# Optimization experiments

Hardware: AMD Instinct MI355X
Metric: run time of the kernel (lower is better)

## Reference

```python
import jax, jax.numpy as jnp
import numpy as np

B, T, N, F_DIM = 8, 32, 64, 6
D, H, C = 128, 4, 32          # hidden, spatial heads, head dim
L_SP, L_T, TH = 3, 3, 4       # spatial layers, temporal layers, temporal heads
THD = D // TH                 # temporal head dim
E = N * (N - 1)


def _ln(x, g, b, eps=1e-5):
    mu = x.mean(-1, keepdims=True)
    var = ((x - mu) ** 2).mean(-1, keepdims=True)
    return (x - mu) * jax.lax.rsqrt(var + eps) * g + b


def setup_inputs() -> dict:
    key = jax.random.key(0)
    ks = iter(jax.random.split(key, 64))
    r = lambda *s: jax.random.normal(next(ks), s, jnp.float32) * 0.05
    src_n, dst_n = np.nonzero(~np.eye(N, dtype=bool))
    inp = {
        'input_frames': jax.random.normal(next(ks), (B, T, N, F_DIM), jnp.float32),
        'edge_attr_seq': jax.random.uniform(next(ks), (B, T, E, 1), jnp.float32),
        'proj_W': r(F_DIM, D), 'proj_b': r(D),
        'sp_Wq': r(L_SP, D, D), 'sp_bq': r(L_SP, D),
        'sp_Wk': r(L_SP, D, D), 'sp_bk': r(L_SP, D),
        'sp_Wv': r(L_SP, D, D), 'sp_bv': r(L_SP, D),
        'sp_We': r(L_SP, 1, D), 'sp_be': r(L_SP, D),
        'sp_Ws': r(L_SP, D, D), 'sp_bs': r(L_SP, D),
        'sp_lng': jnp.ones((L_SP, D), jnp.float32), 'sp_lnb': jnp.zeros((L_SP, D), jnp.float32),
        'temporal_pos': r(1, 512, D),
        't_Wqkv': r(L_T, D, 3 * D), 't_bqkv': r(L_T, 3 * D),
        't_Wo': r(L_T, D, D), 't_bo': r(L_T, D),
        't_ln1g': jnp.ones((L_T, D), jnp.float32), 't_ln1b': jnp.zeros((L_T, D), jnp.float32),
        't_W1': r(L_T, D, 4 * D), 't_b1': r(L_T, 4 * D),
        't_W2': r(L_T, 4 * D, D), 't_b2': r(L_T, D),
        't_ln2g': jnp.ones((L_T, D), jnp.float32), 't_ln2b': jnp.zeros((L_T, D), jnp.float32),
        'head_W1': r(D, D), 'head_b1': r(D),
        'head_W2': r(D, F_DIM), 'head_b2': r(F_DIM),
        'edge_index': jnp.asarray(np.stack([src_n, dst_n]), jnp.int32),
    }
    return inp


def _forward(input_frames, edge_attr_seq, proj_W, proj_b, sp_Wq, sp_bq, sp_Wk, sp_bk,
             sp_Wv, sp_bv, sp_We, sp_be, sp_Ws, sp_bs, sp_lng, sp_lnb, temporal_pos,
             t_Wqkv, t_bqkv, t_Wo, t_bo, t_ln1g, t_ln1b, t_W1, t_b1, t_W2, t_b2,
             t_ln2g, t_ln2b, head_W1, head_b1, head_W2, head_b2, edge_index):
    BT = B * T
    Nt = BT * N                                       # total batched nodes
    offs = jnp.arange(BT, dtype=edge_index.dtype) * N
    src = (edge_index[0][None, :] + offs[:, None]).reshape(-1)   # (BT*E,)
    dst = (edge_index[1][None, :] + offs[:, None]).reshape(-1)
    ea = edge_attr_seq.reshape(BT * E, 1)
    h = input_frames.reshape(Nt, F_DIM) @ proj_W + proj_b        # (Nt, D)

    scale = 1.0 / jnp.sqrt(jnp.float32(C))
    for l in range(L_SP):
        q = (h @ sp_Wq[l] + sp_bq[l]).reshape(Nt, H, C)
        k = (h @ sp_Wk[l] + sp_bk[l]).reshape(Nt, H, C)
        v = (h @ sp_Wv[l] + sp_bv[l]).reshape(Nt, H, C)
        e = (ea @ sp_We[l] + sp_be[l]).reshape(-1, H, C)         # (Et, H, C)
        kj = k[src] + e
        alpha = (q[dst] * kj).sum(-1) * scale                    # (Et, H)
        amax = jax.ops.segment_max(alpha, dst, num_segments=Nt)
        ae = jnp.exp(alpha - amax[dst])
        asum = jax.ops.segment_sum(ae, dst, num_segments=Nt)
        w = ae / asum[dst]                                       # segment softmax
        msg = (v[src] + e) * w[..., None]
        agg = jax.ops.segment_sum(msg, dst, num_segments=Nt).reshape(Nt, D)
        out = agg + h @ sp_Ws[l] + sp_bs[l]                      # root/skip term
        h = _ln(h + out, sp_lng[l], sp_lnb[l])

    z = h.reshape(B, T, N, D).transpose(0, 2, 1, 3).reshape(B * N, T, D)
    z = z + temporal_pos[:, :T, :]

    causal = jnp.tril(jnp.ones((T, T), bool))
    tscale = 1.0 / jnp.sqrt(jnp.float32(THD))
    for l in range(L_T):
        qkv = z @ t_Wqkv[l] + t_bqkv[l]
        q, k, v = jnp.split(qkv, 3, axis=-1)
        q = q.reshape(B * N, T, TH, THD)
        k = k.reshape(B * N, T, TH, THD)
        v = v.reshape(B * N, T, TH, THD)
        s = jnp.einsum('bqhd,bkhd->bhqk', q, k) * tscale
        s = jnp.where(causal, s, -jnp.inf)
        a = jax.nn.softmax(s, axis=-1)
        o = jnp.einsum('bhqk,bkhd->bqhd', a, v).reshape(B * N, T, D)
        o = o @ t_Wo[l] + t_bo[l]
        z = _ln(z + o, t_ln1g[l], t_ln1b[l])
        f = jax.nn.gelu(z @ t_W1[l] + t_b1[l], approximate=False) @ t_W2[l] + t_b2[l]
        z = _ln(z + f, t_ln2g[l], t_ln2b[l])

    h_last = z[:, -1, :].reshape(B, N, D)
    pred = jax.nn.gelu(h_last @ head_W1 + head_b1, approximate=False) @ head_W2 + head_b2
    return pred                                                  # (B, N, F)


def reference(input_frames, edge_attr_seq, proj_W, proj_b, sp_Wq, sp_bq, sp_Wk, sp_bk,
              sp_Wv, sp_bv, sp_We, sp_be, sp_Ws, sp_bs, sp_lng, sp_lnb, temporal_pos,
              t_Wqkv, t_bqkv, t_Wo, t_bo, t_ln1g, t_ln1b, t_W1, t_b1, t_W2, t_b2,
              t_ln2g, t_ln2b, head_W1, head_b1, head_W2, head_b2, edge_index):
    return _forward(input_frames, edge_attr_seq, proj_W, proj_b, sp_Wq, sp_bq, sp_Wk,
                    sp_bk, sp_Wv, sp_bv, sp_We, sp_be, sp_Ws, sp_bs, sp_lng, sp_lnb,
                    temporal_pos, t_Wqkv, t_bqkv, t_Wo, t_bo, t_ln1g, t_ln1b, t_W1,
                    t_b1, t_W2, t_b2, t_ln2g, t_ln2b, head_W1, head_b1, head_W2,
                    head_b2, edge_index)
```

## Files before the change

kernel.cpp:

```cpp
#include <hip/hip_runtime.h>
#include <hip/hip_bf16.h>
#include <math.h>

typedef __hip_bfloat16 bf16;
typedef short short8 __attribute__((ext_vector_type(8)));
typedef float floatx4 __attribute__((ext_vector_type(4)));

#define B_    8
#define T_    32
#define N_    64
#define F_    6
#define D_    128
#define E_    4032
#define BT_   256
#define BN_   512

__device__ __forceinline__ float gelu_exact(float x) {
    return 0.5f * x * (1.0f + erff(x * 0.70710678118654752f));
}
__device__ __forceinline__ float bfbits2f(short s) {
    unsigned int u = ((unsigned int)(unsigned short)s) << 16;
    return __uint_as_float(u);
}
__device__ __forceinline__ void ld32lds(const bf16* p, float* o) {
    const short8* sp = (const short8*)p;
#pragma unroll
    for (int i = 0; i < 4; i++) {
        short8 s = sp[i];
#pragma unroll
        for (int j = 0; j < 8; j++) o[i * 8 + j] = bfbits2f(s[j]);
    }
}

struct RepackDesc { const float* W; bf16* out; int K, N, ntt, ntoff, L, start; };
struct RepackArgs {
    RepackDesc d[9]; int total;
    const float *bq, *bk, *bv; float* spb;
};

__global__ void k_repack(RepackArgs ra) {
    int gid = blockIdx.x * blockDim.x + threadIdx.x;
    if (gid >= ra.total) {
        int i = gid - ra.total;
        if (i < 3 * 384) {
            int l = i / 384, c = i % 384;
            float v = (c < 128) ? ra.bq[l * 128 + c]
                    : (c < 256) ? ra.bk[l * 128 + c - 128]
                                : ra.bv[l * 128 + c - 256];
            ra.spb[i] = v;
        }
        return;
    }
    int fi = 0;
    while (fi < 8 && gid >= ra.d[fi + 1].start) fi++;
    RepackDesc dd = ra.d[fi];
    int r = gid - dd.start;
    int lane = r & 63; r >>= 6;
    int ntiles = dd.N >> 4;
    int nt = r % ntiles; r /= ntiles;
    int ktiles = dd.K >> 5;
    int kt = r % ktiles;
    int l = r / ktiles;
    int quad = lane >> 4, cc = lane & 15;
    const float* Wl = dd.W + (size_t)l * dd.K * dd.N;
    bf16* o = dd.out + ((((size_t)l * ktiles + kt) * dd.ntt + nt + dd.ntoff) * 64 + lane) * 8;
    int kb = kt * 32 + quad * 8;
    int n = nt * 16 + cc;
#pragma unroll
    for (int j = 0; j < 8; j++)
        o[j] = __float2bfloat16(Wl[(size_t)(kb + j) * dd.N + n]);
}

__global__ __launch_bounds__(512, 1)
void k_spatial3(const float* __restrict__ inp, const float* __restrict__ projW,
                const float* __restrict__ projB,
                const short8* __restrict__ BpQKV, const short8* __restrict__ BpWS,
                const float* __restrict__ spb, const float* __restrict__ bs,
                const float* __restrict__ lng, const float* __restrict__ lnb,
                const float* __restrict__ ea, const float* __restrict__ Weg,
                const float* __restrict__ beg, const float* __restrict__ tpos,
                float* __restrict__ z32g) {
    __shared__ short smem[61312];
    bf16* hb = (bf16*)smem;
    bf16* qk = (bf16*)(smem + 8704);
    float* aggf = (float*)(smem + 8704);
    float* fsm = (float*)(smem + 8704);
    bf16* Vt = (bf16*)(smem + 25600);
    bf16* Ps = (bf16*)(smem + 34816);
    float* EAs = (float*)(smem + 53248);

    int bt = blockIdx.x;
    int tid = threadIdx.x;
    int lane = tid & 63, w = tid >> 6;
    int quad = lane >> 4, col = lane & 15;
    int w4 = w & 3, wh = w >> 2;
    const float scale = 0.17677669529663687f;

    for (int i = tid; i < 896; i += 512)
        fsm[i] = (i < 768) ? projW[i] : projB[i - 768];
    {
        const float* eag = ea + (size_t)bt * E_;
        for (int i = tid; i < E_; i += 512) EAs[i] = eag[i];
    }
    __syncthreads();
    float hreg[32];
    if (w < 4) {
#pragma unroll
        for (int r = 0; r < 4; r++) {
            int n = w * 16 + quad * 4 + r;
            const float* xr = inp + (size_t)(bt * 64 + n) * F_;
            float xin[6];
#pragma unroll
            for (int k2 = 0; k2 < 6; k2++) xin[k2] = xr[k2];
#pragma unroll
            for (int tt = 0; tt < 8; tt++) {
                int c = tt * 16 + col;
                float a = fsm[768 + c];
#pragma unroll
                for (int k2 = 0; k2 < 6; k2++) a = fmaf(xin[k2], fsm[k2 * 128 + c], a);
                hreg[tt * 4 + r] = a;
                hb[n * 136 + c] = __float2bfloat16(a);
            }
        }
    }
    __syncthreads();

    for (int l = 0; l < 3; l++) {
        {
            floatx4 acc[12];
#pragma unroll
            for (int tt = 0; tt < 12; tt++) acc[tt] = (floatx4){0.f, 0.f, 0.f, 0.f};
            const short8* bpl = BpQKV + (size_t)l * 6144;
            for (int kt = 0; kt < 4; kt++) {
                short8 a = *(const short8*)&hb[(w4 * 16 + col) * 136 + kt * 32 + quad * 8];
                const short8* bp = bpl + (size_t)(kt * 24 + wh * 12) * 64 + lane;
#pragma unroll
                for (int tt = 0; tt < 12; tt++)
                    acc[tt] = __builtin_amdgcn_mfma_f32_16x16x32_bf16(a, bp[tt * 64], acc[tt], 0, 0, 0);
            }
            const float* bias = spb + l * 384;
#pragma unroll
            for (int tt = 0; tt < 12; tt++) {
                int c = wh * 192 + tt * 16 + col;
                float bv = bias[c];
#pragma unroll
                for (int r = 0; r < 4; r++) {
                    int row = w4 * 16 + quad * 4 + r;
                    bf16 v = __float2bfloat16(acc[tt][r] + bv);
                    if (c < 256) qk[row * 264 + c] = v;
                    else         Vt[(c - 256) * 72 + row] = v;
                }
            }
        }
        __syncthreads();
        int h = w4, half = wh;
        int hoff = h * 32;
        const float* Wel = Weg + l * 128 + hoff;
        const float* bel = beg + l * 128 + hoff;
        float qWe;
        {
            int dst = half * 32 + (lane & 31);
            float qr[32];
            ld32lds(&qk[dst * 264 + hoff], qr);
            float s0 = 0.f, s1 = 0.f, s2 = 0.f, s3 = 0.f;
#pragma unroll
            for (int c2 = 0; c2 < 32; c2 += 4) {
                s0 = fmaf(qr[c2], Wel[c2], s0);
                s1 = fmaf(qr[c2 + 1], Wel[c2 + 1], s1);
                s2 = fmaf(qr[c2 + 2], Wel[c2 + 2], s2);
                s3 = fmaf(qr[c2 + 3], Wel[c2 + 3], s3);
            }
            qWe = (s0 + s1) + (s2 + s3);
        }
        float s[2][4][4], ev[2][4][4];
        {
            short8 aA[2], bB[4];
#pragma unroll
            for (int mtl = 0; mtl < 2; mtl++)
                aA[mtl] = *(const short8*)&qk[((half * 2 + mtl) * 16 + col) * 264 + hoff + quad * 8];
#pragma unroll
            for (int nt = 0; nt < 4; nt++)
                bB[nt] = *(const short8*)&qk[(nt * 16 + col) * 264 + 128 + hoff + quad * 8];
#pragma unroll
            for (int mtl = 0; mtl < 2; mtl++)
#pragma unroll
                for (int nt = 0; nt < 4; nt++) {
                    floatx4 acc = (floatx4){0.f, 0.f, 0.f, 0.f};
                    acc = __builtin_amdgcn_mfma_f32_16x16x32_bf16(aA[mtl], bB[nt], acc, 0, 0, 0);
#pragma unroll
                    for (int r = 0; r < 4; r++) s[mtl][nt][r] = acc[r];
                }
        }
        __syncthreads();
        float ls[2][4], ae[2][4], inv[2][4];
#pragma unroll
        for (int mtl = 0; mtl < 2; mtl++)
#pragma unroll
            for (int r = 0; r < 4; r++) {
                int m = half * 32 + mtl * 16 + quad * 4 + r;
                float qWeR = __shfl(qWe, mtl * 16 + quad * 4 + r, 64);
                float rmax = -1e30f;
#pragma unroll
                for (int nt = 0; nt < 4; nt++) {
                    int n = nt * 16 + col;
                    bool diag = (m == n);
                    int eid = diag ? 0 : (n * 63 + m - (m > n ? 1 : 0));
                    float eav = diag ? 0.f : EAs[eid];
                    ev[mtl][nt][r] = eav;
                    float al = diag ? -1e30f
                                    : scale * (s[mtl][nt][r] + eav * qWeR);
                    s[mtl][nt][r] = al;
                    rmax = fmaxf(rmax, al);
                }
#pragma unroll
                for (int mk2 = 1; mk2 <= 8; mk2 <<= 1)
                    rmax = fmaxf(rmax, __shfl_xor(rmax, mk2, 64));
                float lsum = 0.f, aesum = 0.f;
#pragma unroll
                for (int nt = 0; nt < 4; nt++) {
                    float p = __expf(s[mtl][nt][r] - rmax);
                    s[mtl][nt][r] = p;
                    lsum += p;
                    aesum = fmaf(p, ev[mtl][nt][r], aesum);
                }
#pragma unroll
                for (int mk2 = 1; mk2 <= 8; mk2 <<= 1) {
                    lsum += __shfl_xor(lsum, mk2, 64);
                    aesum += __shfl_xor(aesum, mk2, 64);
                }
                ls[mtl][r] = lsum;
                ae[mtl][r] = aesum;
                inv[mtl][r] = 1.0f / lsum;
            }
        bf16* PsH = Ps + h * 4608;
        floatx4 oacc[2][2];
#pragma unroll
        for (int mtl = 0; mtl < 2; mtl++)
#pragma unroll
            for (int ntB = 0; ntB < 2; ntB++) oacc[mtl][ntB] = (floatx4){0.f, 0.f, 0.f, 0.f};
#pragma unroll
        for (int p = 0; p < 2; p++) {
#pragma unroll
            for (int mtl = 0; mtl < 2; mtl++)
#pragma unroll
                for (int q2 = 0; q2 < 2; q2++) {
                    int nl = q2 * 16 + col;
                    int base0 = (half * 32 + mtl * 16 + quad * 4) * 72 + ((nl >> 3) * 2) * 8 + (nl & 7);
#pragma unroll
                    for (int r = 0; r < 4; r++) {
                        float p_ = s[mtl][2 * p + q2][r];
                        bf16 hi = __float2bfloat16(p_);
                        bf16 lo = __float2bfloat16(p_ - bfbits2f(*(short*)&hi));
                        PsH[base0 + r * 72] = hi;
                        PsH[base0 + r * 72 + 8] = lo;
                    }
                }
            short8 aPh[2], aPl[2], bV[2];
#pragma unroll
            for (int mtl = 0; mtl < 2; mtl++) {
                int rb = (half * 32 + mtl * 16 + col) * 72 + quad * 16;
                aPh[mtl] = *(const short8*)&PsH[rb];
                aPl[mtl] = *(const short8*)&PsH[rb + 8];
            }
#pragma unroll
            for (int ntB = 0; ntB < 2; ntB++)
                bV[ntB] = *(const short8*)&Vt[(hoff + ntB * 16 + col) * 72 + p * 32 + quad * 8];
#pragma unroll
            for (int mtl = 0; mtl < 2; mtl++)
#pragma unroll
                for (int ntB = 0; ntB < 2; ntB++) {
                    oacc[mtl][ntB] = __builtin_amdgcn_mfma_f32_16x16x32_bf16(aPh[mtl], bV[ntB], oacc[mtl][ntB], 0, 0, 0);
                    oacc[mtl][ntB] = __builtin_amdgcn_mfma_f32_16x16x32_bf16(aPl[mtl], bV[ntB], oacc[mtl][ntB], 0, 0, 0);
                }
        }
#pragma unroll
        for (int mtl = 0; mtl < 2; mtl++)
#pragma unroll
            for (int ntB = 0; ntB < 2; ntB++) {
                int c = hoff + ntB * 16 + col;
                float Wc = Wel[ntB * 16 + col];
                float bc = bel[ntB * 16 + col];
#pragma unroll
                for (int r = 0; r < 4; r++) {
                    int m = half * 32 + mtl * 16 + quad * 4 + r;
                    aggf[m * 128 + c] = fmaf(fmaf(ae[mtl][r], Wc, oacc[mtl][ntB][r]),
                                             inv[mtl][r], bc);
                }
            }
        __syncthreads();
        if (w < 4) {
            floatx4 acc2[8];
#pragma unroll
            for (int tt = 0; tt < 8; tt++) acc2[tt] = (floatx4){0.f, 0.f, 0.f, 0.f};
            const short8* bpl = BpWS + (size_t)l * 2048;
            for (int kt = 0; kt < 4; kt++) {
                short8 a = *(const short8*)&hb[(w * 16 + col) * 136 + kt * 32 + quad * 8];
                const short8* bp = bpl + (size_t)(kt * 8) * 64 + lane;
#pragma unroll
                for (int tt = 0; tt < 8; tt++)
                    acc2[tt] = __builtin_amdgcn_mfma_f32_16x16x32_bf16(a, bp[tt * 64], acc2[tt], 0, 0, 0);
            }
            const float* bsl = bs + l * 128;
            float vv[32], rs[4] = {0.f, 0.f, 0.f, 0.f};
#pragma unroll
            for (int tt = 0; tt < 8; tt++) {
                int c = tt * 16 + col;
                float bv = bsl[c];
#pragma unroll
                for (int r = 0; r < 4; r++) {
                    int row = w * 16 + quad * 4 + r;
                    float v = acc2[tt][r] + bv + aggf[row * 128 + c] + hreg[tt * 4 + r];
                    vv[tt * 4 + r] = v;
                    rs[r] += v;
                }
            }
#pragma unroll
            for (int m = 1; m <= 8; m <<= 1)
#pragma unroll
                for (int r = 0; r < 4; r++) rs[r] += __shfl_xor(rs[r], m, 64);
            float mean[4], vs[4] = {0.f, 0.f, 0.f, 0.f};
#pragma unroll
            for (int r = 0; r < 4; r++) mean[r] = rs[r] * (1.0f / 128.0f);
#pragma unroll
            for (int i = 0; i < 32; i++) {
                float d = vv[i] - mean[i & 3];
                vv[i] = d;
                vs[i & 3] += d * d;
            }
#pragma unroll
            for (int m = 1; m <= 8; m <<= 1)
#pragma unroll
                for (int r = 0; r < 4; r++) vs[r] += __shfl_xor(vs[r], m, 64);
            float inv2[4];
#pragma unroll
            for (int r = 0; r < 4; r++) inv2[r] = rsqrtf(vs[r] * (1.0f / 128.0f) + 1e-5f);
            const float* gl = lng + l * 128;
            const float* bl = lnb + l * 128;
            if (l < 2) {
#pragma unroll
                for (int tt = 0; tt < 8; tt++) {
                    int c = tt * 16 + col;
                    float gc = gl[c], bc = bl[c];
#pragma unroll
                    for (int r = 0; r < 4; r++) {
                        float y = vv[tt * 4 + r] * inv2[r] * gc + bc;
                        int n = w * 16 + quad * 4 + r;
                        hreg[tt * 4 + r] = y;
                        hb[n * 136 + c] = __float2bfloat16(y);
                    }
                }
            } else {
                int b = bt >> 5, t_ = bt & 31;
#pragma unroll
                for (int tt = 0; tt < 8; tt++) {
                    int c = tt * 16 + col;
                    float gc = gl[c], bc = bl[c], pc = tpos[t_ * 128 + c];
#pragma unroll
                    for (int r = 0; r < 4; r++) {
                        float y = vv[tt * 4 + r] * inv2[r] * gc + bc;
                        int n = w * 16 + quad * 4 + r;
                        z32g[((size_t)(b * 64 + n) * 32 + t_) * 128 + c] = y + pc;
                    }
                }
            }
        }
        __syncthreads();
    }
}

__global__ __launch_bounds__(512, 4)
void k_temporal3(const float* __restrict__ z32g,
                 const short8* __restrict__ BpQKV, const short8* __restrict__ BpWO,
                 const short8* __restrict__ BpW1, const short8* __restrict__ BpW2,
                 const float* __restrict__ bqkv, const float* __restrict__ bo,
                 const float* __restrict__ ln1g, const float* __restrict__ ln1b,
                 const float* __restrict__ b1, const float* __restrict__ b2,
                 const float* __restrict__ ln2g, const float* __restrict__ ln2b,
                 bf16* __restrict__ zlastb) {
    __shared__ short smem[32000];
    bf16* zb  = (bf16*)smem;
    bf16* qk  = (bf16*)(smem + 4352);
    bf16* Ps  = (bf16*)(smem + 12800);
    bf16* Vt  = (bf16*)(smem + 22016);
    bf16* o16 = (bf16*)(smem + 27136);
    float* lnp = (float*)(smem + 31488);
    bf16* f1  = (bf16*)(smem + 4352);

    int bn = blockIdx.x;
    int tid = threadIdx.x;
    int lane = tid & 63, w = tid >> 6;
    int quad = lane >> 4, col = lane & 15;
    int mt = w & 1, cq = w >> 1;
    const float scale = 0.17677669529663687f;

    for (int i = tid; i < 4096; i += 512) {
        float v = z32g[(size_t)bn * 4096 + i];
        zb[(i >> 7) * 136 + (i & 127)] = __float2bfloat16(v);
    }
    float zreg[8];
#pragma unroll
    for (int t2 = 0; t2 < 2; t2++)
#pragma unroll
        for (int r = 0; r < 4; r++)
            zreg[t2 * 4 + r] = z32g[(size_t)bn * 4096 +
                                    (mt * 16 + quad * 4 + r) * 128 + cq * 32 + t2 * 16 + col];
    __syncthreads();

    for (int l = 0; l < 3; l++) {
        {
            floatx4 acc[6];
#pragma unroll
            for (int tt = 0; tt < 6; tt++) acc[tt] = (floatx4){0.f, 0.f, 0.f, 0.f};
            const short8* bpl = BpQKV + (size_t)l * 6144;
            for (int kt = 0; kt < 4; kt++) {
                short8 a = *(const short8*)&zb[(mt * 16 + col) * 136 + kt * 32 + quad * 8];
                const short8* bp = bpl + (size_t)(kt * 24 + cq * 6) * 64 + lane;
#pragma unroll
                for (int tt = 0; tt < 6; tt++)
                    acc[tt] = __builtin_amdgcn_mfma_f32_16x16x32_bf16(a, bp[tt * 64], acc[tt], 0, 0, 0);
            }
            const float* bias = bqkv + l * 384;
#pragma unroll
            for (int tt = 0; tt < 6; tt++) {
                int c = cq * 96 + tt * 16 + col;
                float bv = bias[c];
#pragma unroll
                for (int r = 0; r < 4; r++) {
                    int row = mt * 16 + quad * 4 + r;
                    bf16 v = __float2bfloat16(acc[tt][r] + bv);
                    if (c < 256) qk[row * 264 + c] = v;
                    else         Vt[(c - 256) * 40 + row] = v;
                }
            }
        }
        __syncthreads();
        {
            int h = w & 3, mh = w >> 2;
            int hoff = h * 32;
            bf16* PsH = Ps + (h * 2 + mh) * 1152;
            float s[2][4];
            short8 aA = *(const short8*)&qk[(mh * 16 + col) * 264 + hoff + quad * 8];
            short8 bB[2];
#pragma unroll
            for (int nt = 0; nt < 2; nt++)
                bB[nt] = *(const short8*)&qk[(nt * 16 + col) * 264 + 128 + hoff + quad * 8];
#pragma unroll
            for (int nt = 0; nt < 2; nt++) {
                floatx4 acc = (floatx4){0.f, 0.f, 0.f, 0.f};
                acc = __builtin_amdgcn_mfma_f32_16x16x32_bf16(aA, bB[nt], acc, 0, 0, 0);
#pragma unroll
                for (int r = 0; r < 4; r++) s[nt][r] = acc[r];
            }
            float inv[4];
#pragma unroll
            for (int r = 0; r < 4; r++) {
                int m = mh * 16 + quad * 4 + r;
                float rmax = -1e30f;
#pragma unroll
                for (int nt = 0; nt < 2; nt++) {
                    int n = nt * 16 + col;
                    float al = (n > m) ? -1e30f : s[nt][r] * scale;
                    s[nt][r] = al;
                    rmax = fmaxf(rmax, al);
                }
#pragma unroll
                for (int mk2 = 1; mk2 <= 8; mk2 <<= 1)
                    rmax = fmaxf(rmax, __shfl_xor(rmax, mk2, 64));
                float lsum = 0.f;
#pragma unroll
                for (int nt = 0; nt < 2; nt++) {
                    float p = __expf(s[nt][r] - rmax);
                    s[nt][r] = p;
                    lsum += p;
                }
#pragma unroll
                for (int mk2 = 1; mk2 <= 8; mk2 <<= 1)
                    lsum += __shfl_xor(lsum, mk2, 64);
                inv[r] = 1.0f / lsum;
            }
#pragma unroll
            for (int nt = 0; nt < 2; nt++) {
                int n = nt * 16 + col;
                int base0 = (quad * 4) * 72 + ((n >> 3) * 2) * 8 + (n & 7);
#pragma unroll
                for (int r = 0; r < 4; r++) {
                    float p_ = s[nt][r];
                    bf16 hi = __float2bfloat16(p_);
                    bf16 lo = __float2bfloat16(p_ - bfbits2f(*(short*)&hi));
                    PsH[base0 + r * 72] = hi;
                    PsH[base0 + r * 72 + 8] = lo;
                }
            }
            floatx4 oacc[2];
#pragma unroll
            for (int nt = 0; nt < 2; nt++) oacc[nt] = (floatx4){0.f, 0.f, 0.f, 0.f};
            short8 aPh = *(const short8*)&PsH[col * 72 + quad * 16];
            short8 aPl = *(const short8*)&PsH[col * 72 + quad * 16 + 8];
            short8 bV[2];
#pragma unroll
            for (int nt = 0; nt < 2; nt++)
                bV[nt] = *(const short8*)&Vt[(hoff + nt * 16 + col) * 40 + quad * 8];
#pragma unroll
            for (int nt = 0; nt < 2; nt++) {
                oacc[nt] = __builtin_amdgcn_mfma_f32_16x16x32_bf16(aPh, bV[nt], oacc[nt], 0, 0, 0);
                oacc[nt] = __builtin_amdgcn_mfma_f32_16x16x32_bf16(aPl, bV[nt], oacc[nt], 0, 0, 0);
            }
#pragma unroll
            for (int nt = 0; nt < 2; nt++) {
                int c = hoff + nt * 16 + col;
#pragma unroll
                for (int r = 0; r < 4; r++)
                    o16[(mh * 16 + quad * 4 + r) * 136 + c] =
                        __float2bfloat16(oacc[nt][r] * inv[r]);
            }
        }
        __syncthreads();
        {
            floatx4 acc2[2];
#pragma unroll
            for (int tt = 0; tt < 2; tt++) acc2[tt] = (floatx4){0.f, 0.f, 0.f, 0.f};
            const short8* bpl = BpWO + (size_t)l * 2048;
            for (int kt = 0; kt < 4; kt++) {
                short8 a = *(const short8*)&o16[(mt * 16 + col) * 136 + kt * 32 + quad * 8];
                const short8* bp = bpl + (size_t)(kt * 8 + cq * 2) * 64 + lane;
#pragma unroll
                for (int tt = 0; tt < 2; tt++)
                    acc2[tt] = __builtin_amdgcn_mfma_f32_16x16x32_bf16(a, bp[tt * 64], acc2[tt], 0, 0, 0);
            }
            const float* bol = bo + l * 128;
            float vv[8], rs[4] = {0.f, 0.f, 0.f, 0.f}, rq[4] = {0.f, 0.f, 0.f, 0.f};
#pragma unroll
            for (int tt = 0; tt < 2; tt++) {
                int c = cq * 32 + tt * 16 + col;
                float bv = bol[c];
#pragma unroll
                for (int r = 0; r < 4; r++) {
                    float v = acc2[tt][r] + bv + zreg[tt * 4 + r];
                    vv[tt * 4 + r] = v;
                    rs[r] += v;
                    rq[r] = fmaf(v, v, rq[r]);
                }
            }
#pragma unroll
            for (int m = 1; m <= 8; m <<= 1)
#pragma unroll
                for (int r = 0; r < 4; r++) {
                    rs[r] += __shfl_xor(rs[r], m, 64);
                    rq[r] += __shfl_xor(rq[r], m, 64);
                }
            if (col == 0) {
#pragma unroll
                for (int r = 0; r < 4; r++) {
                    int row = mt * 16 + quad * 4 + r;
                    lnp[(cq * 32 + row) * 2] = rs[r];
                    lnp[(cq * 32 + row) * 2 + 1] = rq[r];
                }
            }
            __syncthreads();
            const float* gl = ln1g + l * 128;
            const float* bl = ln1b + l * 128;
#pragma unroll
            for (int r = 0; r < 4; r++) {
                int row = mt * 16 + quad * 4 + r;
                float sm = 0.f, sq = 0.f;
#pragma unroll
                for (int q2 = 0; q2 < 4; q2++) {
                    sm += lnp[(q2 * 32 + row) * 2];
                    sq += lnp[(q2 * 32 + row) * 2 + 1];
                }
                float mean = sm * (1.0f / 128.0f);
                float var = sq * (1.0f / 128.0f) - mean * mean;
                float iv = rsqrtf(var + 1e-5f);
#pragma unroll
                for (int tt = 0; tt < 2; tt++) {
                    int c = cq * 32 + tt * 16 + col;
                    float y = (vv[tt * 4 + r] - mean) * iv * gl[c] + bl[c];
                    zreg[tt * 4 + r] = y;
                    zb[row * 136 + c] = __float2bfloat16(y);
                }
            }
        }
        __syncthreads();
        {
            floatx4 acc3[8];
#pragma unroll
            for (int tt = 0; tt < 8; tt++) acc3[tt] = (floatx4){0.f, 0.f, 0.f, 0.f};
            const short8* bpl = BpW1 + (size_t)l * 8192;
            for (int kt = 0; kt < 4; kt++) {
                short8 a = *(const short8*)&zb[(mt * 16 + col) * 136 + kt * 32 + quad * 8];
                const short8* bp = bpl + (size_t)(kt * 32 + cq * 8) * 64 + lane;
#pragma unroll
                for (int tt = 0; tt < 8; tt++)
                    acc3[tt] = __builtin_amdgcn_mfma_f32_16x16x32_bf16(a, bp[tt * 64], acc3[tt], 0, 0, 0);
            }
            const float* b1l = b1 + l * 512;
#pragma unroll
            for (int tt = 0; tt < 8; tt++) {
                int c = cq * 128 + tt * 16 + col;
                float bv = b1l[c];
#pragma unroll
                for (int r = 0; r < 4; r++) {
                    float v = gelu_exact(acc3[tt][r] + bv);
                    f1[(mt * 16 + quad * 4 + r) * 520 + c] = __float2bfloat16(v);
                }
            }
        }
        __syncthreads();
        {
            floatx4 acc4[2];
#pragma unroll
            for (int tt = 0; tt < 2; tt++) acc4[tt] = (floatx4){0.f, 0.f, 0.f, 0.f};
            const short8* bpl = BpW2 + (size_t)l * 8192;
            for (int kt = 0; kt < 16; kt++) {
                short8 a = *(const short8*)&f1[(mt * 16 + col) * 520 + kt * 32 + quad * 8];
                const short8* bp = bpl + (size_t)(kt * 8 + cq * 2) * 64 + lane;
#pragma unroll
                for (int tt = 0; tt < 2; tt++)
                    acc4[tt] = __builtin_amdgcn_mfma_f32_16x16x32_bf16(a, bp[tt * 64], acc4[tt], 0, 0, 0);
            }
            const float* b2l = b2 + l * 128;
            float vv[8], rs[4] = {0.f, 0.f, 0.f, 0.f}, rq[4] = {0.f, 0.f, 0.f, 0.f};
#pragma unroll
            for (int tt = 0; tt < 2; tt++) {
                int c = cq * 32 + tt * 16 + col;
                float bv = b2l[c];
#pragma unroll
                for (int r = 0; r < 4; r++) {
                    float v = acc4[tt][r] + bv + zreg[tt * 4 + r];
                    vv[tt * 4 + r] = v;
                    rs[r] += v;
                    rq[r] = fmaf(v, v, rq[r]);
                }
            }
#pragma unroll
            for (int m = 1; m <= 8; m <<= 1)
#pragma unroll
                for (int r = 0; r < 4; r++) {
                    rs[r] += __shfl_xor(rs[r], m, 64);
                    rq[r] += __shfl_xor(rq[r], m, 64);
                }
            if (col == 0) {
#pragma unroll
                for (int r = 0; r < 4; r++) {
                    int row = mt * 16 + quad * 4 + r;
                    lnp[(cq * 32 + row) * 2] = rs[r];
                    lnp[(cq * 32 + row) * 2 + 1] = rq[r];
                }
            }
            __syncthreads();
            const float* gl = ln2g + l * 128;
            const float* bl = ln2b + l * 128;
#pragma unroll
            for (int r = 0; r < 4; r++) {
                int row = mt * 16 + quad * 4 + r;
                float sm = 0.f, sq = 0.f;
#pragma unroll
                for (int q2 = 0; q2 < 4; q2++) {
                    sm += lnp[(q2 * 32 + row) * 2];
                    sq += lnp[(q2 * 32 + row) * 2 + 1];
                }
                float mean = sm * (1.0f / 128.0f);
                float var = sq * (1.0f / 128.0f) - mean * mean;
                float iv = rsqrtf(var + 1e-5f);
#pragma unroll
                for (int tt = 0; tt < 2; tt++) {
                    int c = cq * 32 + tt * 16 + col;
                    float y = (vv[tt * 4 + r] - mean) * iv * gl[c] + bl[c];
                    zreg[tt * 4 + r] = y;
                    if (l < 2) zb[row * 136 + c] = __float2bfloat16(y);
                    else if (row == 31) zlastb[(size_t)bn * 128 + c] = __float2bfloat16(y);
                }
            }
        }
        __syncthreads();
    }
}

__global__ __launch_bounds__(256)
void k_head(const bf16* __restrict__ zlastb, const short8* __restrict__ BpHW1,
            const float* __restrict__ b1, const float* __restrict__ W2,
            const float* __restrict__ b2, float* __restrict__ out) {
    __shared__ bf16 h1[16 * 136];
    int blk = blockIdx.x;
    int tid = threadIdx.x;
    int lane = tid & 63, w = tid >> 6;
    int quad = lane >> 4, col = lane & 15;
    {
        floatx4 acc[2];
        acc[0] = (floatx4){0.f, 0.f, 0.f, 0.f};
        acc[1] = (floatx4){0.f, 0.f, 0.f, 0.f};
        const short8* Ap = (const short8*)(zlastb + (size_t)(blk * 16 + col) * 128) + quad;
        for (int kt = 0; kt < 4; kt++) {
            short8 a = Ap[kt * 4];
            const short8* bp = BpHW1 + (size_t)(kt * 8 + w * 2) * 64 + lane;
            acc[0] = __builtin_amdgcn_mfma_f32_16x16x32_bf16(a, bp[0], acc[0], 0, 0, 0);
            acc[1] = __builtin_amdgcn_mfma_f32_16x16x32_bf16(a, bp[64], acc[1], 0, 0, 0);
        }
#pragma unroll
        for (int tt = 0; tt < 2; tt++) {
            int c = w * 32 + tt * 16 + col;
            float bv = b1[c];
#pragma unroll
            for (int r = 0; r < 4; r++)
                h1[(quad * 4 + r) * 136 + c] = __float2bfloat16(gelu_exact(acc[tt][r] + bv));
        }
    }
    __syncthreads();
    if (tid < 96) {
        int row = tid / 6, c = tid % 6;
        float a0 = 0.f, a1 = 0.f, a2 = 0.f, a3 = 0.f;
        const bf16* hr = &h1[row * 136];
#pragma unroll 8
        for (int k = 0; k < 128; k += 4) {
            a0 = fmaf(bfbits2f(*(const short*)&hr[k]),     W2[k * 6 + c], a0);
            a1 = fmaf(bfbits2f(*(const short*)&hr[k + 1]), W2[(k + 1) * 6 + c], a1);
            a2 = fmaf(bfbits2f(*(const short*)&hr[k + 2]), W2[(k + 2) * 6 + c], a2);
            a3 = fmaf(bfbits2f(*(const short*)&hr[k + 3]), W2[(k + 3) * 6 + c], a3);
        }
        out[(size_t)(blk * 16 + row) * 6 + c] = (a0 + a1) + (a2 + a3) + b2[c];
    }
}

extern "C" void kernel_launch(void* const* d_in, const int* in_sizes, int n_in,
                              void* d_out, int out_size, void* d_ws, size_t ws_size,
                              hipStream_t stream) {
    const float* input_frames = (const float*)d_in[0];
    const float* edge_attr    = (const float*)d_in[1];
    const float* proj_W  = (const float*)d_in[2];
    const float* proj_b  = (const float*)d_in[3];
    const float* sp_Wq   = (const float*)d_in[4];
    const float* sp_bq   = (const float*)d_in[5];
    const float* sp_Wk   = (const float*)d_in[6];
    const float* sp_bk   = (const float*)d_in[7];
    const float* sp_Wv   = (const float*)d_in[8];
    const float* sp_bv   = (const float*)d_in[9];
    const float* sp_We   = (const float*)d_in[10];
    const float* sp_be   = (const float*)d_in[11];
    const float* sp_Ws   = (const float*)d_in[12];
    const float* sp_bs   = (const float*)d_in[13];
    const float* sp_lng  = (const float*)d_in[14];
    const float* sp_lnb  = (const float*)d_in[15];
    const float* tpos    = (const float*)d_in[16];
    const float* t_Wqkv  = (const float*)d_in[17];
    const float* t_bqkv  = (const float*)d_in[18];
    const float* t_Wo    = (const float*)d_in[19];
    const float* t_bo    = (const float*)d_in[20];
    const float* t_ln1g  = (const float*)d_in[21];
    const float* t_ln1b  = (const float*)d_in[22];
    const float* t_W1    = (const float*)d_in[23];
    const float* t_b1    = (const float*)d_in[24];
    const float* t_W2    = (const float*)d_in[25];
    const float* t_b2    = (const float*)d_in[26];
    const float* t_ln2g  = (const float*)d_in[27];
    const float* t_ln2b  = (const float*)d_in[28];
    const float* head_W1 = (const float*)d_in[29];
    const float* head_b1 = (const float*)d_in[30];
    const float* head_W2 = (const float*)d_in[31];
    const float* head_b2 = (const float*)d_in[32];

    float* f     = (float*)d_ws;
    float* z32g  = f;
    bf16*  zlastb = (bf16*)(f + (1u << 21));
    float* spb   = f + (1u << 21) + 65536;
    bf16* BpBase = (bf16*)(f + (1u << 21) + 65536 + 2048);
    bf16* BpSPQKV = BpBase;
    bf16* BpWS    = BpSPQKV + 147456;
    bf16* BpTQKV  = BpWS + 49152;
    bf16* BpWO    = BpTQKV + 147456;
    bf16* BpW1    = BpWO + 49152;
    bf16* BpW2    = BpW1 + 196608;
    bf16* BpHW1   = BpW2 + 196608;

    RepackArgs ra;
    int s = 0;
    auto mk = [&](int i, const float* W, bf16* out, int K, int N, int ntt, int ntoff, int L) {
        ra.d[i] = {W, out, K, N, ntt, ntoff, L, s};
        s += L * (K >> 5) * (N >> 4) * 64;
    };
    mk(0, sp_Wq, BpSPQKV, 128, 128, 24, 0, 3);
    mk(1, sp_Wk, BpSPQKV, 128, 128, 24, 8, 3);
    mk(2, sp_Wv, BpSPQKV, 128, 128, 24, 16, 3);
    mk(3, sp_Ws, BpWS, 128, 128, 8, 0, 3);
    mk(4, t_Wqkv, BpTQKV, 128, 384, 24, 0, 3);
    mk(5, t_Wo, BpWO, 128, 128, 8, 0, 3);
    mk(6, t_W1, BpW1, 128, 512, 32, 0, 3);
    mk(7, t_W2, BpW2, 512, 128, 8, 0, 3);
    mk(8, head_W1, BpHW1, 128, 128, 8, 0, 1);
    ra.total = s;
    ra.bq = sp_bq; ra.bk = sp_bk; ra.bv = sp_bv; ra.spb = spb;
    k_repack<<<(s + 1152 + 255) / 256, 256, 0, stream>>>(ra);

    k_spatial3<<<BT_, 512, 0, stream>>>(
        input_frames, proj_W, proj_b,
        (const short8*)BpSPQKV, (const short8*)BpWS,
        spb, sp_bs, sp_lng, sp_lnb, edge_attr, sp_We, sp_be, tpos, z32g);

    k_temporal3<<<BN_, 512, 0, stream>>>(
        z32g, (const short8*)BpTQKV, (const short8*)BpWO,
        (const short8*)BpW1, (const short8*)BpW2,
        t_bqkv, t_bo, t_ln1g, t_ln1b, t_b1, t_b2, t_ln2g, t_ln2b, zlastb);

    k_head<<<32, 256, 0, stream>>>(zlastb, (const short8*)BpHW1, head_b1,
                                   head_W2, head_b2, (float*)d_out);
}
```

Before: 279.9 us.

## Process two sequences per temporal block to reuse weight fragments across both

```diff
diff --git a/kernel.cpp b/kernel.cpp
--- a/kernel.cpp
+++ b/kernel.cpp
@@ -368,7 +368,7 @@
     }
 }
 
-__global__ __launch_bounds__(512, 4)
+__global__ __launch_bounds__(512, 2)
 void k_temporal3(const float* __restrict__ z32g,
                  const short8* __restrict__ BpQKV, const short8* __restrict__ BpWO,
                  const short8* __restrict__ BpW1, const short8* __restrict__ BpW2,
@@ -377,47 +377,57 @@
                  const float* __restrict__ b1, const float* __restrict__ b2,
                  const float* __restrict__ ln2g, const float* __restrict__ ln2b,
                  bf16* __restrict__ zlastb) {
-    __shared__ short smem[32000];
+    __shared__ short smem[64000];
     bf16* zb  = (bf16*)smem;
-    bf16* qk  = (bf16*)(smem + 4352);
-    bf16* Ps  = (bf16*)(smem + 12800);
-    bf16* Vt  = (bf16*)(smem + 22016);
-    bf16* o16 = (bf16*)(smem + 27136);
-    float* lnp = (float*)(smem + 31488);
-    bf16* f1  = (bf16*)(smem + 4352);
-
-    int bn = blockIdx.x;
+    bf16* qk  = (bf16*)(smem + 8704);
+    bf16* Ps  = (bf16*)(smem + 25600);
+    bf16* Vt  = (bf16*)(smem + 44032);
+    bf16* o16 = (bf16*)(smem + 54272);
+    float* lnp = (float*)(smem + 62976);
+    bf16* f1  = (bf16*)(smem + 8704);
+
+    int bn0 = blockIdx.x * 2;
     int tid = threadIdx.x;
     int lane = tid & 63, w = tid >> 6;
     int quad = lane >> 4, col = lane & 15;
-    int mt = w & 1, cq = w >> 1;
+    int sq = w & 1, cq = w >> 1;
     const float scale = 0.17677669529663687f;
 
-    for (int i = tid; i < 4096; i += 512) {
-        float v = z32g[(size_t)bn * 4096 + i];
-        zb[(i >> 7) * 136 + (i & 127)] = __float2bfloat16(v);
+    for (int i = tid; i < 8192; i += 512) {
+        int s = i >> 12, j = i & 4095;
+        float v = z32g[(size_t)(bn0 + s) * 4096 + j];
+        zb[s * 4352 + (j >> 7) * 136 + (j & 127)] = __float2bfloat16(v);
     }
-    float zreg[8];
-#pragma unroll
-    for (int t2 = 0; t2 < 2; t2++)
-#pragma unroll
-        for (int r = 0; r < 4; r++)
-            zreg[t2 * 4 + r] = z32g[(size_t)bn * 4096 +
-                                    (mt * 16 + quad * 4 + r) * 128 + cq * 32 + t2 * 16 + col];
+    float zreg[16];
+#pragma unroll
+    for (int mt = 0; mt < 2; mt++)
+#pragma unroll
+        for (int t2 = 0; t2 < 2; t2++)
+#pragma unroll
+            for (int r = 0; r < 4; r++)
+                zreg[mt * 8 + t2 * 4 + r] =
+                    z32g[(size_t)(bn0 + sq) * 4096 +
+                         (mt * 16 + quad * 4 + r) * 128 + cq * 32 + t2 * 16 + col];
     __syncthreads();
 
     for (int l = 0; l < 3; l++) {
         {
-            floatx4 acc[6];
-#pragma unroll
-            for (int tt = 0; tt < 6; tt++) acc[tt] = (floatx4){0.f, 0.f, 0.f, 0.f};
+            floatx4 acc[2][6];
+#pragma unroll
+            for (int mt = 0; mt < 2; mt++)
+#pragma unroll
+                for (int tt = 0; tt < 6; tt++) acc[mt][tt] = (floatx4){0.f, 0.f, 0.f, 0.f};
             const short8* bpl = BpQKV + (size_t)l * 6144;
             for (int kt = 0; kt < 4; kt++) {
-                short8 a = *(const short8*)&zb[(mt * 16 + col) * 136 + kt * 32 + quad * 8];
+                short8 a0 = *(const short8*)&zb[sq * 4352 + col * 136 + kt * 32 + quad * 8];
+                short8 a1 = *(const short8*)&zb[sq * 4352 + (16 + col) * 136 + kt * 32 + quad * 8];
                 const short8* bp = bpl + (size_t)(kt * 24 + cq * 6) * 64 + lane;
 #pragma unroll
-                for (int tt = 0; tt < 6; tt++)
-                    acc[tt] = __builtin_amdgcn_mfma_f32_16x16x32_bf16(a, bp[tt * 64], acc[tt], 0, 0, 0);
+                for (int tt = 0; tt < 6; tt++) {
+                    short8 b = bp[tt * 64];
+                    acc[0][tt] = __builtin_amdgcn_mfma_f32_16x16x32_bf16(a0, b, acc[0][tt], 0, 0, 0);
+                    acc[1][tt] = __builtin_amdgcn_mfma_f32_16x16x32_bf16(a1, b, acc[1][tt], 0, 0, 0);
+                }
             }
             const float* bias = bqkv + l * 384;
 #pragma unroll
@@ -425,173 +435,217 @@
                 int c = cq * 96 + tt * 16 + col;
                 float bv = bias[c];
 #pragma unroll
-                for (int r = 0; r < 4; r++) {
-                    int row = mt * 16 + quad * 4 + r;
-                    bf16 v = __float2bfloat16(acc[tt][r] + bv);
-                    if (c < 256) qk[row * 264 + c] = v;
-                    else         Vt[(c - 256) * 40 + row] = v;
-                }
+                for (int mt = 0; mt < 2; mt++)
+#pragma unroll
+                    for (int r = 0; r < 4; r++) {
+                        int row = mt * 16 + quad * 4 + r;
+                        bf16 v = __float2bfloat16(acc[mt][tt][r] + bv);
+                        if (c < 256) qk[sq * 8448 + row * 264 + c] = v;
+                        else         Vt[sq * 5120 + (c - 256) * 40 + row] = v;
+                    }
             }
         }
         __syncthreads();
         {
-            int h = w & 3, mh = w >> 2;
-            int hoff = h * 32;
-            bf16* PsH = Ps + (h * 2 + mh) * 1152;
-            float s[2][4];
-            short8 aA = *(const short8*)&qk[(mh * 16 + col) * 264 + hoff + quad * 8];
-            short8 bB[2];
+            int hoff = cq * 32;
+            bf16* PsH = Ps + w * 2304;
+            const bf16* qkS = qk + sq * 8448;
+            float s[2][2][4];
+            short8 aA[2], bB[2];
+#pragma unroll
+            for (int mt = 0; mt < 2; mt++)
+                aA[mt] = *(const short8*)&qkS[(mt * 16 + col) * 264 + hoff + quad * 8];
 #pragma unroll
             for (int nt = 0; nt < 2; nt++)
-                bB[nt] = *(const short8*)&qk[(nt * 16 + col) * 264 + 128 + hoff + quad * 8];
-#pragma unroll
-            for (int nt = 0; nt < 2; nt++) {
-                floatx4 acc = (floatx4){0.f, 0.f, 0.f, 0.f};
-                acc = __builtin_amdgcn_mfma_f32_16x16x32_bf16(aA, bB[nt], acc, 0, 0, 0);
-#pragma unroll
-                for (int r = 0; r < 4; r++) s[nt][r] = acc[r];
-            }
-            float inv[4];
-#pragma unroll
-            for (int r = 0; r < 4; r++) {
-                int m = mh * 16 + quad * 4 + r;
-                float rmax = -1e30f;
+                bB[nt] = *(const short8*)&qkS[(nt * 16 + col) * 264 + 128 + hoff + quad * 8];
+#pragma unroll
+            for (int mt = 0; mt < 2; mt++)
+#pragma unroll
+                for (int nt = 0; nt < 2; nt++) {
+                    floatx4 acc = (floatx4){0.f, 0.f, 0.f, 0.f};
+                    acc = __builtin_amdgcn_mfma_f32_16x16x32_bf16(aA[mt], bB[nt], acc, 0, 0, 0);
+#pragma unroll
+                    for (int r = 0; r < 4; r++) s[mt][nt][r] = acc[r];
+                }
+            float inv[2][4];
+#pragma unroll
+            for (int mt = 0; mt < 2; mt++)
+#pragma unroll
+                for (int r = 0; r < 4; r++) {
+                    int m = mt * 16 + quad * 4 + r;
+                    float rmax = -1e30f;
+#pragma unroll
+                    for (int nt = 0; nt < 2; nt++) {
+                        int n = nt * 16 + col;
+                        float al = (n > m) ? -1e30f : s[mt][nt][r] * scale;
+                        s[mt][nt][r] = al;
+                        rmax = fmaxf(rmax, al);
+                    }
+#pragma unroll
+                    for (int mk2 = 1; mk2 <= 8; mk2 <<= 1)
+                        rmax = fmaxf(rmax, __shfl_xor(rmax, mk2, 64));
+                    float lsum = 0.f;
+#pragma unroll
+                    for (int nt = 0; nt < 2; nt++) {
+                        float p = __expf(s[mt][nt][r] - rmax);
+                        s[mt][nt][r] = p;
+                        lsum += p;
+                    }
+#pragma unroll
+                    for (int mk2 = 1; mk2 <= 8; mk2 <<= 1)
+                        lsum += __shfl_xor(lsum, mk2, 64);
+                    inv[mt][r] = 1.0f / lsum;
+                }
+#pragma unroll
+            for (int mt = 0; mt < 2; mt++)
 #pragma unroll
                 for (int nt = 0; nt < 2; nt++) {
                     int n = nt * 16 + col;
-                    float al = (n > m) ? -1e30f : s[nt][r] * scale;
-                    s[nt][r] = al;
-                    rmax = fmaxf(rmax, al);
-                }
-#pragma unroll
-                for (int mk2 = 1; mk2 <= 8; mk2 <<= 1)
-                    rmax = fmaxf(rmax, __shfl_xor(rmax, mk2, 64));
-                float lsum = 0.f;
+                    int base0 = (mt * 16 + quad * 4) * 72 + ((n >> 3) * 2) * 8 + (n & 7);
+#pragma unroll
+                    for (int r = 0; r < 4; r++) {
+                        float p_ = s[mt][nt][r];
+                        bf16 hi = __float2bfloat16(p_);
+                        bf16 lo = __float2bfloat16(p_ - bfbits2f(*(short*)&hi));
+                        PsH[base0 + r * 72] = hi;
+                        PsH[base0 + r * 72 + 8] = lo;
+                    }
+                }
+            floatx4 oacc[2][2];
+#pragma unroll
+            for (int mt = 0; mt < 2; mt++)
+#pragma unroll
+                for (int nt = 0; nt < 2; nt++) oacc[mt][nt] = (floatx4){0.f, 0.f, 0.f, 0.f};
+            short8 aPh[2], aPl[2], bV[2];
+#pragma unroll
+            for (int mt = 0; mt < 2; mt++) {
+                int rb = (mt * 16 + col) * 72 + quad * 16;
+                aPh[mt] = *(const short8*)&PsH[rb];
+                aPl[mt] = *(const short8*)&PsH[rb + 8];
+            }
+#pragma unroll
+            for (int nt = 0; nt < 2; nt++)
+                bV[nt] = *(const short8*)&Vt[sq * 5120 + (hoff + nt * 16 + col) * 40 + quad * 8];
+#pragma unroll
+            for (int mt = 0; mt < 2; mt++)
 #pragma unroll
                 for (int nt = 0; nt < 2; nt++) {
-                    float p = __expf(s[nt][r] - rmax);
-                    s[nt][r] = p;
-                    lsum += p;
-                }
-#pragma unroll
-                for (int mk2 = 1; mk2 <= 8; mk2 <<= 1)
-                    lsum += __shfl_xor(lsum, mk2, 64);
-                inv[r] = 1.0f / lsum;
-            }
-#pragma unroll
-            for (int nt = 0; nt < 2; nt++) {
-                int n = nt * 16 + col;
-                int base0 = (quad * 4) * 72 + ((n >> 3) * 2) * 8 + (n & 7);
-#pragma unroll
-                for (int r = 0; r < 4; r++) {
-                    float p_ = s[nt][r];
-                    bf16 hi = __float2bfloat16(p_);
-                    bf16 lo = __float2bfloat16(p_ - bfbits2f(*(short*)&hi));
-                    PsH[base0 + r * 72] = hi;
-                    PsH[base0 + r * 72 + 8] = lo;
-                }
-            }
-            floatx4 oacc[2];
-#pragma unroll
-            for (int nt = 0; nt < 2; nt++) oacc[nt] = (floatx4){0.f, 0.f, 0.f, 0.f};
-            short8 aPh = *(const short8*)&PsH[col * 72 + quad * 16];
-            short8 aPl = *(const short8*)&PsH[col * 72 + quad * 16 + 8];
-            short8 bV[2];
-#pragma unroll
-            for (int nt = 0; nt < 2; nt++)
-                bV[nt] = *(const short8*)&Vt[(hoff + nt * 16 + col) * 40 + quad * 8];
-#pragma unroll
-            for (int nt = 0; nt < 2; nt++) {
-                oacc[nt] = __builtin_amdgcn_mfma_f32_16x16x32_bf16(aPh, bV[nt], oacc[nt], 0, 0, 0);
-                oacc[nt] = __builtin_amdgcn_mfma_f32_16x16x32_bf16(aPl, bV[nt], oacc[nt], 0, 0, 0);
-            }
-#pragma unroll
-            for (int nt = 0; nt < 2; nt++) {
-                int c = hoff + nt * 16 + col;
-#pragma unroll
-                for (int r = 0; r < 4; r++)
-                    o16[(mh * 16 + quad * 4 + r) * 136 + c] =
-                        __float2bfloat16(oacc[nt][r] * inv[r]);
-            }
+                    oacc[mt][nt] = __builtin_amdgcn_mfma_f32_16x16x32_bf16(aPh[mt], bV[nt], oacc[mt][nt], 0, 0, 0);
+                    oacc[mt][nt] = __builtin_amdgcn_mfma_f32_16x16x32_bf16(aPl[mt], bV[nt], oacc[mt][nt], 0, 0, 0);
+                }
+#pragma unroll
+            for (int mt = 0; mt < 2; mt++)
+#pragma unroll
+                for (int nt = 0; nt < 2; nt++) {
+                    int c = hoff + nt * 16 + col;
+#pragma unroll
+                    for (int r = 0; r < 4; r++)
+                        o16[sq * 4352 + (mt * 16 + quad * 4 + r) * 136 + c] =
+                            __float2bfloat16(oacc[mt][nt][r] * inv[mt][r]);
+                }
         }
         __syncthreads();
         {
-            floatx4 acc2[2];
-#pragma unroll
-            for (int tt = 0; tt < 2; tt++) acc2[tt] = (floatx4){0.f, 0.f, 0.f, 0.f};
+            floatx4 acc2[2][2];
+#pragma unroll
+            for (int mt = 0; mt < 2; mt++)
+#pragma unroll
+                for (int tt = 0; tt < 2; tt++) acc2[mt][tt] = (floatx4){0.f, 0.f, 0.f, 0.f};
             const short8* bpl = BpWO + (size_t)l * 2048;
             for (int kt = 0; kt < 4; kt++) {
-                short8 a = *(const short8*)&o16[(mt * 16 + col) * 136 + kt * 32 + quad * 8];
+                short8 a0 = *(const short8*)&o16[sq * 4352 + col * 136 + kt * 32 + quad * 8];
+                short8 a1 = *(const short8*)&o16[sq * 4352 + (16 + col) * 136 + kt * 32 + quad * 8];
                 const short8* bp = bpl + (size_t)(kt * 8 + cq * 2) * 64 + lane;
 #pragma unroll
-                for (int tt = 0; tt < 2; tt++)
-                    acc2[tt] = __builtin_amdgcn_mfma_f32_16x16x32_bf16(a, bp[tt * 64], acc2[tt], 0, 0, 0);
+                for (int tt = 0; tt < 2; tt++) {
+                    short8 b = bp[tt * 64];
+                    acc2[0][tt] = __builtin_amdgcn_mfma_f32_16x16x32_bf16(a0, b, acc2[0][tt], 0, 0, 0);
+                    acc2[1][tt] = __builtin_amdgcn_mfma_f32_16x16x32_bf16(a1, b, acc2[1][tt], 0, 0, 0);
+                }
             }
             const float* bol = bo + l * 128;
-            float vv[8], rs[4] = {0.f, 0.f, 0.f, 0.f}, rq[4] = {0.f, 0.f, 0.f, 0.f};
-#pragma unroll
-            for (int tt = 0; tt < 2; tt++) {
-                int c = cq * 32 + tt * 16 + col;
-                float bv = bol[c];
-#pragma unroll
-                for (int r = 0; r < 4; r++) {
-                    float v = acc2[tt][r] + bv + zreg[tt * 4 + r];
-                    vv[tt * 4 + r] = v;
-                    rs[r] += v;
-                    rq[r] = fmaf(v, v, rq[r]);
-                }
-            }
+            float vv[16], rs[2][4], rq[2][4];
+#pragma unroll
+            for (int mt = 0; mt < 2; mt++)
+#pragma unroll
+                for (int r = 0; r < 4; r++) { rs[mt][r] = 0.f; rq[mt][r] = 0.f; }
+#pragma unroll
+            for (int mt = 0; mt < 2; mt++)
+#pragma unroll
+                for (int tt = 0; tt < 2; tt++) {
+                    int c = cq * 32 + tt * 16 + col;
+                    float bv = bol[c];
+#pragma unroll
+                    for (int r = 0; r < 4; r++) {
+                        float v = acc2[mt][tt][r] + bv + zreg[mt * 8 + tt * 4 + r];
+                        vv[mt * 8 + tt * 4 + r] = v;
+                        rs[mt][r] += v;
+                        rq[mt][r] = fmaf(v, v, rq[mt][r]);
+                    }
+                }
 #pragma unroll
             for (int m = 1; m <= 8; m <<= 1)
 #pragma unroll
-                for (int r = 0; r < 4; r++) {
-                    rs[r] += __shfl_xor(rs[r], m, 64);
-                    rq[r] += __shfl_xor(rq[r], m, 64);
-                }
+                for (int mt = 0; mt < 2; mt++)
+#pragma unroll
+                    for (int r = 0; r < 4; r++) {
+                        rs[mt][r] += __shfl_xor(rs[mt][r], m, 64);
+                        rq[mt][r] += __shfl_xor(rq[mt][r], m, 64);
+                    }
             if (col == 0) {
 #pragma unroll
-                for (int r = 0; r < 4; r++) {
-                    int row = mt * 16 + quad * 4 + r;
-                    lnp[(cq * 32 + row) * 2] = rs[r];
-                    lnp[(cq * 32 + row) * 2 + 1] = rq[r];
-                }
+                for (int mt = 0; mt < 2; mt++)
+#pragma unroll
+                    for (int r = 0; r < 4; r++) {
+                        int row = mt * 16 + quad * 4 + r;
+                        lnp[((sq * 4 + cq) * 32 + row) * 2] = rs[mt][r];
+                        lnp[((sq * 4 + cq) * 32 + row) * 2 + 1] = rq[mt][r];
+                    }
             }
             __syncthreads();
             const float* gl = ln1g + l * 128;
             const float* bl = ln1b + l * 128;
 #pragma unroll
-            for (int r = 0; r < 4; r++) {
-                int row = mt * 16 + quad * 4 + r;
-                float sm = 0.f, sq = 0.f;
-#pragma unroll
-                for (int q2 = 0; q2 < 4; q2++) {
-                    sm += lnp[(q2 * 32 + row) * 2];
-                    sq += lnp[(q2 * 32 + row) * 2 + 1];
-                }
-                float mean = sm * (1.0f / 128.0f);
-                float var = sq * (1.0f / 128.0f) - mean * mean;
-                float iv = rsqrtf(var + 1e-5f);
-#pragma unroll
-                for (int tt = 0; tt < 2; tt++) {
-                    int c = cq * 32 + tt * 16 + col;
-                    float y = (vv[tt * 4 + r] - mean) * iv * gl[c] + bl[c];
-                    zreg[tt * 4 + r] = y;
-                    zb[row * 136 + c] = __float2bfloat16(y);
-                }
-            }
+            for (int mt = 0; mt < 2; mt++)
+#pragma unroll
+                for (int r = 0; r < 4; r++) {
+                    int row = mt * 16 + quad * 4 + r;
+                    float sm = 0.f, sqs = 0.f;
+#pragma unroll
+                    for (int q2 = 0; q2 < 4; q2++) {
+                        sm += lnp[((sq * 4 + q2) * 32 + row) * 2];
+                        sqs += lnp[((sq * 4 + q2) * 32 + row) * 2 + 1];
+                    }
+                    float mean = sm * (1.0f / 128.0f);
+                    float var = sqs * (1.0f / 128.0f) - mean * mean;
+                    float iv = rsqrtf(var + 1e-5f);
+#pragma unroll
+                    for (int tt = 0; tt < 2; tt++) {
+                        int c = cq * 32 + tt * 16 + col;
+                        float y = (vv[mt * 8 + tt * 4 + r] - mean) * iv * gl[c] + bl[c];
+                        zreg[mt * 8 + tt * 4 + r] = y;
+                        zb[sq * 4352 + row * 136 + c] = __float2bfloat16(y);
+                    }
+                }
         }
         __syncthreads();
         {
-            floatx4 acc3[8];
-#pragma unroll
-            for (int tt = 0; tt < 8; tt++) acc3[tt] = (floatx4){0.f, 0.f, 0.f, 0.f};
+            floatx4 acc3[2][8];
+#pragma unroll
+            for (int mt = 0; mt < 2; mt++)
+#pragma unroll
+                for (int tt = 0; tt < 8; tt++) acc3[mt][tt] = (floatx4){0.f, 0.f, 0.f, 0.f};
             const short8* bpl = BpW1 + (size_t)l * 8192;
             for (int kt = 0; kt < 4; kt++) {
-                short8 a = *(const short8*)&zb[(mt * 16 + col) * 136 + kt * 32 + quad * 8];
+                short8 a0 = *(const short8*)&zb[sq * 4352 + col * 136 + kt * 32 + quad * 8];
+                short8 a1 = *(const short8*)&zb[sq * 4352 + (16 + col) * 136 + kt * 32 + quad * 8];
                 const short8* bp = bpl + (size_t)(kt * 32 + cq * 8) * 64 + lane;
 #pragma unroll
-                for (int tt = 0; tt < 8; tt++)
-                    acc3[tt] = __builtin_amdgcn_mfma_f32_16x16x32_bf16(a, bp[tt * 64], acc3[tt], 0, 0, 0);
+                for (int tt = 0; tt < 8; tt++) {
+                    short8 b = bp[tt * 64];
+                    acc3[0][tt] = __builtin_amdgcn_mfma_f32_16x16x32_bf16(a0, b, acc3[0][tt], 0, 0, 0);
+                    acc3[1][tt] = __builtin_amdgcn_mfma_f32_16x16x32_bf16(a1, b, acc3[1][tt], 0, 0, 0);
+                }
             }
             const float* b1l = b1 + l * 512;
 #pragma unroll
@@ -599,78 +653,99 @@
                 int c = cq * 128 + tt * 16 + col;
                 float bv = b1l[c];
 #pragma unroll
-                for (int r = 0; r < 4; r++) {
-                    float v = gelu_exact(acc3[tt][r] + bv);
-                    f1[(mt * 16 + quad * 4 + r) * 520 + c] = __float2bfloat16(v);
-                }
+                for (int mt = 0; mt < 2; mt++)
+#pragma unroll
+                    for (int r = 0; r < 4; r++) {
+                        float v = gelu_exact(acc3[mt][tt][r] + bv);
+                        f1[sq * 16640 + (mt * 16 + quad * 4 + r) * 520 + c] = __float2bfloat16(v);
+                    }
             }
         }
         __syncthreads();
         {
-            floatx4 acc4[2];
-#pragma unroll
-            for (int tt = 0; tt < 2; tt++) acc4[tt] = (floatx4){0.f, 0.f, 0.f, 0.f};
+            floatx4 acc4[2][2];
+#pragma unroll
+            for (int mt = 0; mt < 2; mt++)
+#pragma unroll
+                for (int tt = 0; tt < 2; tt++) acc4[mt][tt] = (floatx4){0.f, 0.f, 0.f, 0.f};
             const short8* bpl = BpW2 + (size_t)l * 8192;
             for (int kt = 0; kt < 16; kt++) {
-                short8 a = *(const short8*)&f1[(mt * 16 + col) * 520 + kt * 32 + quad * 8];
+                short8 a0 = *(const short8*)&f1[sq * 16640 + col * 520 + kt * 32 + quad * 8];
+                short8 a1 = *(const short8*)&f1[sq * 16640 + (16 + col) * 520 + kt * 32 + quad * 8];
                 const short8* bp = bpl + (size_t)(kt * 8 + cq * 2) * 64 + lane;
 #pragma unroll
-                for (int tt = 0; tt < 2; tt++)
-                    acc4[tt] = __builtin_amdgcn_mfma_f32_16x16x32_bf16(a, bp[tt * 64], acc4[tt], 0, 0, 0);
+                for (int tt = 0; tt < 2; tt++) {
+                    short8 b = bp[tt * 64];
+                    acc4[0][tt] = __builtin_amdgcn_mfma_f32_16x16x32_bf16(a0, b, acc4[0][tt], 0, 0, 0);
+                    acc4[1][tt] = __builtin_amdgcn_mfma_f32_16x16x32_bf16(a1, b, acc4[1][tt], 0, 0, 0);
+                }
             }
             const float* b2l = b2 + l * 128;
-            float vv[8], rs[4] = {0.f, 0.f, 0.f, 0.f}, rq[4] = {0.f, 0.f, 0.f, 0.f};
-#pragma unroll
-            for (int tt = 0; tt < 2; tt++) {
-                int c = cq * 32 + tt * 16 + col;
-                float bv = b2l[c];
-#pragma unroll
-                for (int r = 0; r < 4; r++) {
-                    float v = acc4[tt][r] + bv + zreg[tt * 4 + r];
-                    vv[tt * 4 + r] = v;
-                    rs[r] += v;
-                    rq[r] = fmaf(v, v, rq[r]);
-                }
-            }
+            float vv[16], rs[2][4], rq[2][4];
+#pragma unroll
+            for (int mt = 0; mt < 2; mt++)
+#pragma unroll
+                for (int r = 0; r < 4; r++) { rs[mt][r] = 0.f; rq[mt][r] = 0.f; }
+#pragma unroll
+            for (int mt = 0; mt < 2; mt++)
+#pragma unroll
+                for (int tt = 0; tt < 2; tt++) {
+                    int c = cq * 32 + tt * 16 + col;
+                    float bv = b2l[c];
+#pragma unroll
+                    for (int r = 0; r < 4; r++) {
+                        float v = acc4[mt][tt][r] + bv + zreg[mt * 8 + tt * 4 + r];
+                        vv[mt * 8 + tt * 4 + r] = v;
+                        rs[mt][r] += v;
+                        rq[mt][r] = fmaf(v, v, rq[mt][r]);
+                    }
+                }
 #pragma unroll
             for (int m = 1; m <= 8; m <<= 1)
 #pragma unroll
-                for (int r = 0; r < 4; r++) {
-                    rs[r] += __shfl_xor(rs[r], m, 64);
-                    rq[r] += __shfl_xor(rq[r], m, 64);
-                }
+                for (int mt = 0; mt < 2; mt++)
+#pragma unroll
+                    for (int r = 0; r < 4; r++) {
+                        rs[mt][r] += __shfl_xor(rs[mt][r], m, 64);
+                        rq[mt][r] += __shfl_xor(rq[mt][r], m, 64);
+                    }
             if (col == 0) {
 #pragma unroll
-                for (int r = 0; r < 4; r++) {
-                    int row = mt * 16 + quad * 4 + r;
-                    lnp[(cq * 32 + row) * 2] = rs[r];
-                    lnp[(cq * 32 + row) * 2 + 1] = rq[r];
-                }
+                for (int mt = 0; mt < 2; mt++)
+#pragma unroll
+                    for (int r = 0; r < 4; r++) {
+                        int row = mt * 16 + quad * 4 + r;
+                        lnp[((sq * 4 + cq) * 32 + row) * 2] = rs[mt][r];
+                        lnp[((sq * 4 + cq) * 32 + row) * 2 + 1] = rq[mt][r];
+                    }
             }
             __syncthreads();
             const float* gl = ln2g + l * 128;
             const float* bl = ln2b + l * 128;
 #pragma unroll
-            for (int r = 0; r < 4; r++) {
-                int row = mt * 16 + quad * 4 + r;
-                float sm = 0.f, sq = 0.f;
-#pragma unroll
-                for (int q2 = 0; q2 < 4; q2++) {
-                    sm += lnp[(q2 * 32 + row) * 2];
-                    sq += lnp[(q2 * 32 + row) * 2 + 1];
-                }
-                float mean = sm * (1.0f / 128.0f);
-                float var = sq * (1.0f / 128.0f) - mean * mean;
-                float iv = rsqrtf(var + 1e-5f);
-#pragma unroll
-                for (int tt = 0; tt < 2; tt++) {
-                    int c = cq * 32 + tt * 16 + col;
-                    float y = (vv[tt * 4 + r] - mean) * iv * gl[c] + bl[c];
-                    zreg[tt * 4 + r] = y;
-                    if (l < 2) zb[row * 136 + c] = __float2bfloat16(y);
-                    else if (row == 31) zlastb[(size_t)bn * 128 + c] = __float2bfloat16(y);
-                }
-            }
+            for (int mt = 0; mt < 2; mt++)
+#pragma unroll
+                for (int r = 0; r < 4; r++) {
+                    int row = mt * 16 + quad * 4 + r;
+                    float sm = 0.f, sqs = 0.f;
+#pragma unroll
+                    for (int q2 = 0; q2 < 4; q2++) {
+                        sm += lnp[((sq * 4 + q2) * 32 + row) * 2];
+                        sqs += lnp[((sq * 4 + q2) * 32 + row) * 2 + 1];
+                    }
+                    float mean = sm * (1.0f / 128.0f);
+                    float var = sqs * (1.0f / 128.0f) - mean * mean;
+                    float iv = rsqrtf(var + 1e-5f);
+#pragma unroll
+                    for (int tt = 0; tt < 2; tt++) {
+                        int c = cq * 32 + tt * 16 + col;
+                        float y = (vv[mt * 8 + tt * 4 + r] - mean) * iv * gl[c] + bl[c];
+                        zreg[mt * 8 + tt * 4 + r] = y;
+                        if (l < 2) zb[sq * 4352 + row * 136 + c] = __float2bfloat16(y);
+                        else if (row == 31)
+                            zlastb[(size_t)(bn0 + sq) * 128 + c] = __float2bfloat16(y);
+                    }
+                }
         }
         __syncthreads();
     }
@@ -795,7 +870,7 @@
         (const short8*)BpSPQKV, (const short8*)BpWS,
         spb, sp_bs, sp_lng, sp_lnb, edge_attr, sp_We, sp_be, tpos, z32g);
 
-    k_temporal3<<<BN_, 512, 0, stream>>>(
+    k_temporal3<<<BN_ / 2, 512, 0, stream>>>(
         z32g, (const short8*)BpTQKV, (const short8*)BpWO,
         (const short8*)BpW1, (const short8*)BpW2,
         t_bqkv, t_bo, t_ln1g, t_ln1b, t_b1, t_b2, t_ln2g, t_ln2b, zlastb);
```

Result: slower. 292.7 us (+4.6%).
